# Kernel tuning notes

Measured on AMD Instinct MI355X. Metric: run time of the kernel, lower is better.

The kernel has to match this reference:

```python
import jax, jax.numpy as jnp
import numpy as np

MARKER = 50251
BETA_FLOOR = 0.1
LOCAL_SCALE = 0.3
EPS = 1e-6
WINDOW = 256

B, T, D, H, K, V = 4, 1024, 1024, 16, 64, 64
HD = D // H  # SWA head dim


def setup_inputs() -> dict:
    key = jax.random.key(0)
    ks = jax.random.split(key, 16)
    p = lambda i, shape: jax.random.normal(ks[i], shape, jnp.float32) * 0.02
    return dict(
        x=jax.random.normal(ks[0], (B, T, D), jnp.float32),
        initial_state=jnp.zeros((B, H, K, V), jnp.float32),
        W_k=p(1, (D, H * K)),
        W_v=p(2, (D, H * V)),
        W_gdn_o=p(3, (H * V, D)),
        W_beta=p(4, (D, H)), b_beta=jnp.full((H,), -2.0, jnp.float32),
        W_g=p(5, (D, H)), b_g=jnp.full((H,), 2.0, jnp.float32),
        W_lq=p(6, (D, D)), W_lk=p(7, (D, D)), W_lv=p(8, (D, D)),
        W_swa_o=p(9, (D, D)),
        W_ret_o=p(10, (H * V, D)),
        W_gate=p(11, (D, H)), b_gate=jnp.ones((H,), jnp.float32),
        norm_w=jnp.ones((D,), jnp.float32),
        input_ids=jax.random.randint(ks[12], (B, T), 0, 50257, jnp.int32),
    )


def _delta_scan(k, v, beta, g, S0):
    # gated delta rule:  Sd = g_t * S_{t-1};  S_t = Sd + beta_t * k_t (v_t - k_t Sd);  o_t = k_t S_t
    # k:[B,Tm,H,K]  v:[B,Tm,H,V]  beta,g:[B,Tm,H]  S0:[B,H,K,V]
    def step(S, inp):
        kt, vt, bt, gt = inp  # [B,H,K],[B,H,V],[B,H],[B,H]
        Sd = gt[..., None, None] * S
        err = vt - jnp.einsum('bhk,bhkv->bhv', kt, Sd)
        Sn = Sd + bt[..., None, None] * (kt[..., None] * err[:, :, None, :])
        ot = jnp.einsum('bhk,bhkv->bhv', kt, Sn)
        return Sn, ot
    Sf, o = jax.lax.scan(step, S0, (k.transpose(1, 0, 2, 3), v.transpose(1, 0, 2, 3),
                                    beta.transpose(1, 0, 2), g.transpose(1, 0, 2)))
    return o.transpose(1, 0, 2, 3), Sf  # [B,Tm,H,V], [B,H,K,V]


def _forward(x, initial_state, W_k, W_v, W_gdn_o, W_beta, b_beta, W_g, b_g,
             W_lq, W_lk, W_lv, W_swa_o, W_ret_o, W_gate, b_gate, norm_w, input_ids):
    # RMSNorm
    rms = jnp.sqrt(jnp.mean(x * x, axis=-1, keepdims=True) + EPS)
    xn = x / rms * norm_w

    # shared L2-normalized keys and values
    k_shared = (xn @ W_k).reshape(B, T, H, K)
    k_shared = k_shared / jnp.maximum(jnp.linalg.norm(k_shared, axis=-1, keepdims=True), 1e-12)
    v_full = (xn @ W_v).reshape(B, T, H, V)

    # shifted-value GDN inputs (predict next token's value)
    k = k_shared[:, :-1]
    v = v_full[:, 1:]
    beta = jax.nn.sigmoid(xn[:, :-1] @ W_beta + b_beta)  # [B,T-1,H]
    g = jax.nn.sigmoid(xn[:, :-1] @ W_g + b_g)
    marker = (input_ids[:, :-1] == MARKER)[..., None]
    beta = beta * (BETA_FLOOR + (1.0 - BETA_FLOOR) * marker.astype(beta.dtype))

    o, Sf = _delta_scan(k, v, beta, g, initial_state)
    gdn_out = jnp.concatenate([jnp.zeros((B, 1, H, V), o.dtype), o], axis=1)
    gdn_out = gdn_out.reshape(B, T, H * V) @ W_gdn_o  # [B,T,D]

    # sliding-window attention (fallback masked-softmax path)
    q = (xn @ W_lq).reshape(B, T, H, HD).transpose(0, 2, 1, 3)
    kl = (xn @ W_lk).reshape(B, T, H, HD).transpose(0, 2, 1, 3)
    vl = (xn @ W_lv).reshape(B, T, H, HD).transpose(0, 2, 1, 3)
    scale = K ** (-0.5)
    i = jnp.arange(T)[:, None]
    j = jnp.arange(T)[None, :]
    allowed = (j <= i) & (j >= i - WINDOW)  # causal within window
    attn = jnp.einsum('bhqd,bhkd->bhqk', q, kl) * scale
    attn = jnp.where(allowed, attn, -jnp.inf)
    probs = jax.nn.softmax(attn, axis=-1)
    local = jnp.einsum('bhqk,bhkd->bhqd', probs, vl).transpose(0, 2, 1, 3).reshape(B, T, D)
    local_out = LOCAL_SCALE * (local @ W_swa_o)  # eval mode

    # retrieval from final state with shared keys as queries
    retrieved = jnp.einsum('bhkv,bthk->bthv', Sf, k_shared).reshape(B, T, H * V)
    retrieval_out = retrieved @ W_ret_o
    gate = jax.nn.sigmoid(xn @ W_gate + b_gate)  # [B,T,H]
    retrieval_out = jnp.mean(gate, axis=-1, keepdims=True) * retrieval_out

    return x + gdn_out + local_out + retrieval_out


def reference(x, initial_state, W_k, W_v, W_gdn_o, W_beta, b_beta, W_g, b_g,
              W_lq, W_lk, W_lv, W_swa_o, W_ret_o, W_gate, b_gate, norm_w, input_ids):
    return _forward(x, initial_state, W_k, W_v, W_gdn_o, W_beta, b_beta, W_g, b_g,
                    W_lq, W_lk, W_lv, W_swa_o, W_ret_o, W_gate, b_gate, norm_w, input_ids)
```

## Files before the change

### kernel.cpp

```cpp
#include <hip/hip_runtime.h>
#include <hip/hip_bf16.h>

#define BB 4
#define TT 1024
#define DD 1024
#define HH 16
#define KK 64
#define VV 64
#define WIN 256
#define MARKER_ID 50251
#define PSA 5120
#define PSB 3072
#define NPROJ 5248

typedef short bfrag8 __attribute__((ext_vector_type(8)));
typedef float f32x4 __attribute__((ext_vector_type(4)));

static __device__ __forceinline__ unsigned short f2bf(float f) {
  __hip_bfloat16 h = __float2bfloat16(f);
  union { __hip_bfloat16 h; unsigned short u; } cv;
  cv.h = h;
  return cv.u;
}
static __device__ __forceinline__ float bf2f(unsigned short u) {
  union { unsigned int i; float f; } c;
  c.i = ((unsigned int)u) << 16;
  return c.f;
}
static __device__ __forceinline__ void gld_lds16(const unsigned short* g,
                                                 unsigned short* l) {
  __builtin_amdgcn_global_load_lds(
      (const __attribute__((address_space(1))) void*)g,
      (__attribute__((address_space(3))) void*)l, 16, 0, 0);
}

static __device__ __forceinline__ void rmsnorm_body(
    int row, const float* __restrict__ x, const float* __restrict__ nw,
    unsigned short* __restrict__ xnb, float* red) {
  int tid = threadIdx.x;
  const float4* xr = (const float4*)(x + (size_t)row * DD);
  float4 v = xr[tid];
  float ss = v.x * v.x + v.y * v.y + v.z * v.z + v.w * v.w;
#pragma unroll
  for (int off = 32; off; off >>= 1) ss += __shfl_xor(ss, off);
  int wid = tid >> 6;
  if ((tid & 63) == 0) red[wid] = ss;
  __syncthreads();
  float tot = red[0] + red[1] + red[2] + red[3];
  float inv = 1.0f / sqrtf(tot * (1.0f / DD) + 1e-6f);
  const float4* wr = (const float4*)nw;
  float4 wv = wr[tid];
  ushort4 o;
  o.x = f2bf(v.x * inv * wv.x);
  o.y = f2bf(v.y * inv * wv.y);
  o.z = f2bf(v.z * inv * wv.z);
  o.w = f2bf(v.w * inv * wv.w);
  *(ushort4*)&xnb[(size_t)row * DD + tid * 4] = o;
}

static __device__ __forceinline__ void convert_body(
    int xb, int yb, int zb, const float* W0, const float* W1, const float* W2,
    const float* W3, const float* W4, const float* W5, const float* W6,
    const float* W7, const float* Wb, const float* Wg, const float* Wgt,
    unsigned short* C5, unsigned short* C3, float (*Ts)[68]) {
  int tid = threadIdx.x;
  if (zb == 8) {
    if (xb != 0) return;
    int k0 = yb * 64;
    for (int e = tid; e < 3 * 16 * 64; e += 256) {
      int w = e >> 10;
      int h = (e >> 6) & 15;
      int kk = e & 63;
      const float* Ws = (w == 0) ? Wb : (w == 1) ? Wg : Wgt;
      C5[(size_t)(5120 + w * 16 + h) * 1024 + k0 + kk] =
          f2bf(Ws[(size_t)(k0 + kk) * 16 + h]);
    }
    for (int e = tid; e < 80 * 64; e += 256) {
      int r = e >> 6, kk = e & 63;
      C5[(size_t)(5168 + r) * 1024 + k0 + kk] = 0;
    }
    return;
  }
  const float* W;
  unsigned short* T;
  int stride;
  float scale = 1.f;
  switch (zb) {
    case 0: W = W0; T = C5 + 0 * 1024 * 1024; stride = 1024; break;
    case 1: W = W1; T = C5 + 1 * 1024 * 1024; stride = 1024; break;
    case 2: W = W2; T = C5 + 2 * 1024 * 1024; stride = 1024; break;
    case 3: W = W3; T = C5 + 3 * 1024 * 1024; stride = 1024; break;
    case 4: W = W4; T = C5 + 4 * 1024 * 1024; stride = 1024; break;
    case 5: W = W5; T = C3 + 0; stride = PSB; break;
    case 6: W = W6; T = C3 + 1024; stride = PSB; scale = 0.3f; break;
    default: W = W7; T = C3 + 2048; stride = PSB; break;
  }
  int n0 = xb * 64, k0 = yb * 64;
#pragma unroll
  for (int p = 0; p < 4; ++p) {
    int e = p * 256 + tid;
    int k = e >> 4, nq = e & 15;
    float4 w = *(const float4*)&W[(size_t)(k0 + k) * 1024 + n0 + nq * 4];
    Ts[nq * 4 + 0][k] = w.x;
    Ts[nq * 4 + 1][k] = w.y;
    Ts[nq * 4 + 2][k] = w.z;
    Ts[nq * 4 + 3][k] = w.w;
  }
  __syncthreads();
#pragma unroll
  for (int p = 0; p < 4; ++p) {
    int e = p * 256 + tid;
    int n = e >> 4, kq = e & 15;
    float4 v = *(const float4*)&Ts[n][kq * 4];
    ushort4 u;
    u.x = f2bf(v.x * scale);
    u.y = f2bf(v.y * scale);
    u.z = f2bf(v.z * scale);
    u.w = f2bf(v.w * scale);
    *(ushort4*)&T[(size_t)(n0 + n) * stride + k0 + kq * 4] = u;
  }
}

__global__ __launch_bounds__(256) void prep_kernel(
    const float* __restrict__ x, const float* __restrict__ nw,
    unsigned short* __restrict__ xnb, const float* W0, const float* W1,
    const float* W2, const float* W3, const float* W4, const float* W5,
    const float* W6, const float* W7, const float* Wb, const float* Wg,
    const float* Wgt, unsigned short* C5, unsigned short* C3) {
  __shared__ __align__(16) float Ts[64][68];
  int f = blockIdx.x;
  if (f < 4096) {
    rmsnorm_body(f, x, nw, xnb, &Ts[0][0]);
  } else {
    int c = f - 4096;
    convert_body(c & 15, (c >> 4) & 15, c >> 8, W0, W1, W2, W3, W4, W5, W6, W7,
                 Wb, Wg, Wgt, C5, C3, Ts);
  }
}

__global__ __launch_bounds__(256) void gemm_out_kernel(
    const unsigned short* __restrict__ A, const unsigned short* __restrict__ BT,
    float* __restrict__ C, const float* __restrict__ addp, int M, int N,
    int K) {
  __shared__ unsigned short As[2][128][32];
  __shared__ unsigned short Bs[2][64][32];
  int flat = blockIdx.y * gridDim.x + blockIdx.x;
  int xcd = flat & 7, local = flat >> 3;
  int m0 = (xcd * 4 + (local & 3)) * 128;
  int n0 = (local >> 2) * 64;
  int tid = threadIdx.x;
  int wave = tid >> 6, lane = tid & 63;
  int wm = wave * 32;
  int r16 = lane & 15, quad = lane >> 4;
  int lrow = lane >> 2, lcol = (lane & 3) * 8;

  f32x4 acc[2][4];
#pragma unroll
  for (int i = 0; i < 2; ++i)
#pragma unroll
    for (int j = 0; j < 4; ++j) acc[i][j] = {0.f, 0.f, 0.f, 0.f};

  auto STAGE = [&](int buf, int kt) {
#pragma unroll
    for (int q = 0; q < 2; ++q) {
      int rb = (wave * 2 + q) * 16;
      gld_lds16(&A[(size_t)(m0 + rb + lrow) * K + kt + lcol], &As[buf][rb][0]);
    }
    {
      int rb = wave * 16;
      gld_lds16(&BT[(size_t)(n0 + rb + lrow) * K + kt + lcol], &Bs[buf][rb][0]);
    }
  };
  auto COMPUTE = [&](int buf) {
    bfrag8 af[2], bq[4];
#pragma unroll
    for (int i = 0; i < 2; ++i)
      af[i] = *(const bfrag8*)&As[buf][wm + i * 16 + r16][quad * 8];
#pragma unroll
    for (int j = 0; j < 4; ++j)
      bq[j] = *(const bfrag8*)&Bs[buf][j * 16 + r16][quad * 8];
#pragma unroll
    for (int i = 0; i < 2; ++i)
#pragma unroll
      for (int j = 0; j < 4; ++j)
        acc[i][j] = __builtin_amdgcn_mfma_f32_16x16x32_bf16(af[i], bq[j],
                                                            acc[i][j], 0, 0, 0);
  };

  STAGE(0, 0);
  STAGE(1, 32);
  asm volatile("s_waitcnt vmcnt(3)" ::: "memory");
  __builtin_amdgcn_s_barrier();
  __builtin_amdgcn_sched_barrier(0);

  int cur = 0;
  for (int kt = 64; kt < K; kt += 32) {
    COMPUTE(cur);
    __builtin_amdgcn_s_barrier();
    STAGE(cur, kt);
    asm volatile("s_waitcnt vmcnt(3)" ::: "memory");
    __builtin_amdgcn_s_barrier();
    __builtin_amdgcn_sched_barrier(0);
    cur ^= 1;
  }
  COMPUTE(cur);
  asm volatile("s_waitcnt vmcnt(0)" ::: "memory");
  __builtin_amdgcn_s_barrier();
  __builtin_amdgcn_sched_barrier(0);
  COMPUTE(cur ^ 1);

#pragma unroll
  for (int i = 0; i < 2; ++i) {
#pragma unroll
    for (int r = 0; r < 4; ++r) {
      int row = m0 + wm + i * 16 + quad * 4 + r;
#pragma unroll
      for (int j = 0; j < 4; ++j) {
        int col = n0 + j * 16 + r16;
        size_t idx = (size_t)row * N + col;
        C[idx] = addp[idx] + acc[i][j][r];
      }
    }
  }
}

__global__ __launch_bounds__(256, 4) void gemm_proj_kernel(
    const unsigned short* __restrict__ A, const unsigned short* __restrict__ BT,
    unsigned short* __restrict__ PALL, float* __restrict__ SPRJ) {
  const int K = 1024;
  __shared__ unsigned short As[2][128][32];
  __shared__ unsigned short Bs[2][128][32];
  int flat = blockIdx.y * gridDim.x + blockIdx.x;
  int xcd = flat & 7, local = flat >> 3;
  int mi = local & 3, ni = local >> 2;
  int m0 = (xcd * 4 + mi) * 128;
  int n0 = ni * 128;
  int tid = threadIdx.x;
  int wave = tid >> 6, lane = tid & 63;
  int wm = (wave & 1) * 64, wn = (wave >> 1) * 64;
  int r16 = lane & 15, quad = lane >> 4;
  int lrow = lane >> 2, lcol = (lane & 3) * 8;

  f32x4 acc[4][4];
#pragma unroll
  for (int i = 0; i < 4; ++i)
#pragma unroll
    for (int j = 0; j < 4; ++j) acc[i][j] = {0.f, 0.f, 0.f, 0.f};

#pragma unroll
  for (int q = 0; q < 2; ++q) {
    int rb = (wave * 2 + q) * 16;
    gld_lds16(&A[(size_t)(m0 + rb + lrow) * K + lcol], &As[0][rb][0]);
    gld_lds16(&BT[(size_t)(n0 + rb + lrow) * K + lcol], &Bs[0][rb][0]);
  }
  __syncthreads();

  int cur = 0;
  for (int kt = 32; kt < K; kt += 32) {
#pragma unroll
    for (int q = 0; q < 2; ++q) {
      int rb = (wave * 2 + q) * 16;
      gld_lds16(&A[(size_t)(m0 + rb + lrow) * K + kt + lcol],
                &As[cur ^ 1][rb][0]);
      gld_lds16(&BT[(size_t)(n0 + rb + lrow) * K + kt + lcol],
                &Bs[cur ^ 1][rb][0]);
    }
    bfrag8 af[4], bq[4];
#pragma unroll
    for (int i = 0; i < 4; ++i) {
      af[i] = *(const bfrag8*)&As[cur][wm + i * 16 + r16][quad * 8];
      bq[i] = *(const bfrag8*)&Bs[cur][wn + i * 16 + r16][quad * 8];
    }
#pragma unroll
    for (int i = 0; i < 4; ++i)
#pragma unroll
      for (int j = 0; j < 4; ++j)
        acc[i][j] = __builtin_amdgcn_mfma_f32_16x16x32_bf16(af[i], bq[j],
                                                            acc[i][j], 0, 0, 0);
    __syncthreads();
    cur ^= 1;
  }
  {
    bfrag8 af[4], bq[4];
#pragma unroll
    for (int i = 0; i < 4; ++i) {
      af[i] = *(const bfrag8*)&As[cur][wm + i * 16 + r16][quad * 8];
      bq[i] = *(const bfrag8*)&Bs[cur][wn + i * 16 + r16][quad * 8];
    }
#pragma unroll
    for (int i = 0; i < 4; ++i)
#pragma unroll
      for (int j = 0; j < 4; ++j)
        acc[i][j] = __builtin_amdgcn_mfma_f32_16x16x32_bf16(af[i], bq[j],
                                                            acc[i][j], 0, 0, 0);
  }
  bool gates = (n0 >= 5120);
#pragma unroll
  for (int i = 0; i < 4; ++i) {
#pragma unroll
    for (int r = 0; r < 4; ++r) {
      int row = m0 + wm + i * 16 + quad * 4 + r;
#pragma unroll
      for (int j = 0; j < 4; ++j) {
        int col = n0 + wn + j * 16 + r16;
        if (!gates)
          PALL[(size_t)row * PSA + col] = f2bf(acc[i][j][r]);
        else
          SPRJ[(size_t)row * 128 + col - 5120] = acc[i][j][r];
      }
    }
  }
}

__global__ __launch_bounds__(256) void ng_kernel(
    unsigned short* __restrict__ pall, const float* __restrict__ SPRJ,
    const float* __restrict__ bb, const float* __restrict__ bg,
    const float* __restrict__ bgt, const int* __restrict__ ids,
    float* __restrict__ beta, float* __restrict__ g, float* __restrict__ mg) {
  int f = blockIdx.x;
  if (f < 16384) {
    int w = f * 4 + (threadIdx.x >> 6);
    int lane = threadIdx.x & 63;
    size_t addr = (size_t)(w >> 4) * PSA + (w & 15) * 64 + lane;
    float v = bf2f(pall[addr]);
    float ss = v * v;
#pragma unroll
    for (int off = 32; off; off >>= 1) ss += __shfl_xor(ss, off);
    float n = sqrtf(ss);
    n = fmaxf(n, 1e-12f);
    pall[addr] = f2bf(v / n);
  } else {
    int row = (f - 16384) * 4 + (threadIdx.x >> 6);
    int lane = threadIdx.x & 63;
    if (lane < 48) {
      int h = lane & 15;
      float v = SPRJ[(size_t)row * 128 + lane];
      float bias = (lane < 16) ? bb[h] : (lane < 32) ? bg[h] : bgt[h];
      float s = 1.f / (1.f + __expf(-(v + bias)));
      if (lane < 16) {
        float mk = (ids[row] == MARKER_ID) ? 1.f : 0.1f;
        beta[(size_t)row * 16 + h] = s * mk;
      } else if (lane < 32) {
        g[(size_t)row * 16 + h] = s;
      } else {
        float sum = s;
#pragma unroll
        for (int off = 1; off < 16; off <<= 1) sum += __shfl_xor(sum, off);
        if (lane == 32) mg[row] = sum * (1.f / 16.f);
      }
    }
  }
}

__global__ __launch_bounds__(256) void attn_mfma_kernel(
    const unsigned short* __restrict__ PALL, unsigned short* __restrict__ ACAT) {
  __shared__ unsigned short Qs[64][72];
  __shared__ unsigned short Ks[64][72];
  __shared__ unsigned short Vt[64][72];
  __shared__ unsigned short Ps[64][72];
  int qb = blockIdx.x * 64;
  int bh = blockIdx.y;
  int h = bh & 15, b = bh >> 4;
  int tid = threadIdx.x, lane = tid & 63, wave = tid >> 6;
  int r16 = lane & 15, quad = lane >> 4;
  int m0w = wave * 16;
  const unsigned short* Qg = PALL + (size_t)b * TT * PSA + 2048 + h * 64;
  const unsigned short* Kg = Qg + 1024;
  const unsigned short* Vg = Qg + 2048;
  int sr = tid >> 2, sq = tid & 3;
  int kt0 = qb - (int)WIN;
  if (kt0 < 0) kt0 = 0;

  uint4 kr0, kr1;
  union { uint4 u4[2]; unsigned short s[16]; } vr;
  {
    *(uint4*)&Qs[sr][sq * 16] =
        *(const uint4*)&Qg[(size_t)(qb + sr) * PSA + sq * 16];
    *(uint4*)&Qs[sr][sq * 16 + 8] =
        *(const uint4*)&Qg[(size_t)(qb + sr) * PSA + sq * 16 + 8];
    kr0 = *(const uint4*)&Kg[(size_t)(kt0 + sr) * PSA + sq * 16];
    kr1 = *(const uint4*)&Kg[(size_t)(kt0 + sr) * PSA + sq * 16 + 8];
    vr.u4[0] = *(const uint4*)&Vg[(size_t)(kt0 + sr) * PSA + sq * 16];
    vr.u4[1] = *(const uint4*)&Vg[(size_t)(kt0 + sr) * PSA + sq * 16 + 8];
  }
  __syncthreads();
  bfrag8 af0 = *(const bfrag8*)&Qs[m0w + r16][quad * 8];
  bfrag8 af1 = *(const bfrag8*)&Qs[m0w + r16][quad * 8 + 32];
  {
    *(uint4*)&Ks[sr][sq * 16] = kr0;
    *(uint4*)&Ks[sr][sq * 16 + 8] = kr1;
#pragma unroll
    for (int i = 0; i < 16; ++i) Vt[sq * 16 + i][sr] = vr.s[i];
  }
  __syncthreads();

  float m[4], l[4];
  f32x4 o[4];
#pragma unroll
  for (int r = 0; r < 4; ++r) {
    m[r] = -1e30f;
    l[r] = 0.f;
    o[r] = {0.f, 0.f, 0.f, 0.f};
  }

  for (int kt = kt0; kt <= qb; kt += 64) {
    bool more = (kt + 64 <= qb);
    if (more) {
      kr0 = *(const uint4*)&Kg[(size_t)(kt + 64 + sr) * PSA + sq * 16];
      kr1 = *(const uint4*)&Kg[(size_t)(kt + 64 + sr) * PSA + sq * 16 + 8];
      vr.u4[0] = *(const uint4*)&Vg[(size_t)(kt + 64 + sr) * PSA + sq * 16];
      vr.u4[1] = *(const uint4*)&Vg[(size_t)(kt + 64 + sr) * PSA + sq * 16 + 8];
    }
    f32x4 s[4];
#pragma unroll
    for (int j = 0; j < 4; ++j) s[j] = {0.f, 0.f, 0.f, 0.f};
#pragma unroll
    for (int j = 0; j < 4; ++j) {
      bfrag8 b0 = *(const bfrag8*)&Ks[j * 16 + r16][quad * 8];
      bfrag8 b1 = *(const bfrag8*)&Ks[j * 16 + r16][quad * 8 + 32];
      s[j] = __builtin_amdgcn_mfma_f32_16x16x32_bf16(af0, b0, s[j], 0, 0, 0);
      s[j] = __builtin_amdgcn_mfma_f32_16x16x32_bf16(af1, b1, s[j], 0, 0, 0);
    }
    bool oldest = (kt == qb - (int)WIN);
    bool newest = (kt == qb);
#pragma unroll
    for (int r = 0; r < 4; ++r) {
      int il = m0w + quad * 4 + r;
      float sv[4];
#pragma unroll
      for (int j = 0; j < 4; ++j) {
        int jl = j * 16 + r16;
        float v = s[j][r] * 0.125f;
        if (oldest && jl < il) v = -1e30f;
        if (newest && jl > il) v = -1e30f;
        sv[j] = v;
      }
      float mx = fmaxf(fmaxf(sv[0], sv[1]), fmaxf(sv[2], sv[3]));
#pragma unroll
      for (int off = 1; off < 16; off <<= 1) mx = fmaxf(mx, __shfl_xor(mx, off));
      float mn = fmaxf(m[r], mx);
      float al = __expf(m[r] - mn);
      m[r] = mn;
      float rs = 0.f;
#pragma unroll
      for (int j = 0; j < 4; ++j) {
        float p = __expf(sv[j] - mn);
        rs += p;
        Ps[il][j * 16 + r16] = f2bf(p);
      }
#pragma unroll
      for (int off = 1; off < 16; off <<= 1) rs += __shfl_xor(rs, off);
      l[r] = l[r] * al + rs;
#pragma unroll
      for (int j = 0; j < 4; ++j) o[j][r] *= al;
    }
    bfrag8 pa0 = *(const bfrag8*)&Ps[m0w + r16][quad * 8];
    bfrag8 pa1 = *(const bfrag8*)&Ps[m0w + r16][quad * 8 + 32];
#pragma unroll
    for (int j = 0; j < 4; ++j) {
      bfrag8 v0 = *(const bfrag8*)&Vt[j * 16 + r16][quad * 8];
      bfrag8 v1 = *(const bfrag8*)&Vt[j * 16 + r16][quad * 8 + 32];
      o[j] = __builtin_amdgcn_mfma_f32_16x16x32_bf16(pa0, v0, o[j], 0, 0, 0);
      o[j] = __builtin_amdgcn_mfma_f32_16x16x32_bf16(pa1, v1, o[j], 0, 0, 0);
    }
    if (more) {
      __syncthreads();
      *(uint4*)&Ks[sr][sq * 16] = kr0;
      *(uint4*)&Ks[sr][sq * 16 + 8] = kr1;
#pragma unroll
      for (int i = 0; i < 16; ++i) Vt[sq * 16 + i][sr] = vr.s[i];
      __syncthreads();
    }
  }
#pragma unroll
  for (int r = 0; r < 4; ++r) {
    int row = m0w + quad * 4 + r;
    float inv = 1.f / l[r];
#pragma unroll
    for (int j = 0; j < 4; ++j) {
      ACAT[((size_t)(b * TT + qb + row)) * PSB + 1024 + h * 64 + j * 16 + r16] =
          f2bf(o[j][r] * inv);
    }
  }
}

__global__ __launch_bounds__(256) void scan_phaseA(
    const unsigned short* __restrict__ PALL, const float* __restrict__ beta,
    const float* __restrict__ g, unsigned short* __restrict__ UFg,
    unsigned short* __restrict__ Zg, unsigned short* __restrict__ Pg,
    unsigned short* __restrict__ Qg, float* __restrict__ Ag) {
  __shared__ unsigned short Kc[64][72];
  __shared__ unsigned short KTb[64][72];
  __shared__ float Vc[64][68];
  __shared__ float Msv[64][68];
  __shared__ unsigned short UFT[64][72];
  __shared__ unsigned short ZTl[64][72];
  __shared__ float aArr[64], iaArr[64], bArr[64], baArr[64], sKT[64];
  __shared__ float aCs;

  int c = blockIdx.x, bh = blockIdx.y;
  int b = bh >> 4, h = bh & 15;
  int tc = c * 64;
  int tid = threadIdx.x, lane = tid & 63, wave = tid >> 6;
  int r16 = lane & 15, quad = lane >> 4;
  int m0w = wave * 16;
  size_t bhc = (size_t)bh * 16 + c;

  const unsigned short* kbase = PALL + ((size_t)b * TT) * PSA + h * 64;
  const unsigned short* vbase = kbase + 1024;
  const float* bbase = beta + ((size_t)b * TT) * HH + h;
  const float* gbase = g + ((size_t)b * TT) * HH + h;

  if (tid < 64) {
    int ts = tc + tid;
    bool pad = (ts > 1022);
    float gv = pad ? 1.f : gbase[(size_t)ts * HH];
    float bv = pad ? 0.f : bbase[(size_t)ts * HH];
    float p = gv;
#pragma unroll
    for (int o = 1; o < 64; o <<= 1) {
      float t = __shfl_up(p, o);
      if (lane >= o) p *= t;
    }
    aArr[tid] = p;
    iaArr[tid] = 1.f / p;
    bArr[tid] = bv;
    baArr[tid] = bv * p;
    float aC = __shfl(p, 63);
    sKT[tid] = aC / p;
    if (tid == 0) aCs = aC;
    Ag[bhc * 64 + tid] = p;
  }
  __syncthreads();
  {
    int r = tid >> 2, q = tid & 3;
    int ts = tc + r;
    float skt = sKT[r];
    union { uint4 u4[2]; unsigned short s[16]; } kv;
    kv.u4[0] = *(const uint4*)&kbase[(size_t)ts * PSA + q * 16];
    kv.u4[1] = *(const uint4*)&kbase[(size_t)ts * PSA + q * 16 + 8];
    *(uint4*)&Kc[r][q * 16] = kv.u4[0];
    *(uint4*)&Kc[r][q * 16 + 8] = kv.u4[1];
#pragma unroll
    for (int i = 0; i < 16; ++i)
      KTb[q * 16 + i][r] = f2bf(bf2f(kv.s[i]) * skt);
    if (ts <= 1022) {
      union { uint4 u4[2]; unsigned short s[16]; } vv;
      vv.u4[0] = *(const uint4*)&vbase[(size_t)(ts + 1) * PSA + q * 16];
      vv.u4[1] = *(const uint4*)&vbase[(size_t)(ts + 1) * PSA + q * 16 + 8];
#pragma unroll
      for (int i = 0; i < 16; ++i) Vc[r][q * 16 + i] = bf2f(vv.s[i]);
    } else {
#pragma unroll
      for (int i = 0; i < 16; ++i) Vc[r][q * 16 + i] = 0.f;
    }
  }
  __syncthreads();
  {
    bfrag8 af0 = *(const bfrag8*)&Kc[m0w + r16][quad * 8];
    bfrag8 af1 = *(const bfrag8*)&Kc[m0w + r16][quad * 8 + 32];
    f32x4 acc1[4];
#pragma unroll
    for (int j = 0; j < 4; ++j) acc1[j] = {0.f, 0.f, 0.f, 0.f};
#pragma unroll
    for (int j = 0; j < 4; ++j) {
      bfrag8 k0 = *(const bfrag8*)&Kc[j * 16 + r16][quad * 8];
      bfrag8 k1 = *(const bfrag8*)&Kc[j * 16 + r16][quad * 8 + 32];
      acc1[j] = __builtin_amdgcn_mfma_f32_16x16x32_bf16(af0, k0, acc1[j], 0, 0, 0);
      acc1[j] = __builtin_amdgcn_mfma_f32_16x16x32_bf16(af1, k1, acc1[j], 0, 0, 0);
    }
#pragma unroll
    for (int j = 0; j < 4; ++j) {
#pragma unroll
      for (int r = 0; r < 4; ++r) {
        int row = m0w + quad * 4 + r;
        int col = j * 16 + r16;
        Msv[row][col] =
            (col < row) ? bArr[row] * aArr[row] * iaArr[col] * acc1[j][r] : 0.f;
      }
    }
  }
  __syncthreads();
  if (wave < 2) {
    float u[64];
    if (wave == 0) {
#pragma unroll
      for (int t = 0; t < 64; ++t) u[t] = bArr[t] * Vc[t][lane];
    } else {
#pragma unroll
      for (int t = 0; t < 64; ++t) u[t] = baArr[t] * bf2f(Kc[t][lane]);
    }
#pragma unroll
    for (int t = 1; t < 64; ++t) {
      float a0 = 0.f, a1 = 0.f, a2 = 0.f, a3 = 0.f;
#pragma unroll
      for (int s4 = 0; s4 * 4 < t; ++s4) {
        float4 mr = *(const float4*)&Msv[t][s4 * 4];
        a0 = fmaf(mr.x, u[s4 * 4 + 0], a0);
        a1 = fmaf(mr.y, u[s4 * 4 + 1], a1);
        a2 = fmaf(mr.z, u[s4 * 4 + 2], a2);
        a3 = fmaf(mr.w, u[s4 * 4 + 3], a3);
      }
      u[t] -= (a0 + a1) + (a2 + a3);
    }
    unsigned short* Tls = (wave == 0) ? &UFT[lane][0] : &ZTl[lane][0];
#pragma unroll
    for (int t2 = 0; t2 < 32; ++t2) {
      unsigned int pk = (unsigned int)f2bf(u[2 * t2]) |
                        ((unsigned int)f2bf(u[2 * t2 + 1]) << 16);
      *(unsigned int*)&Tls[2 * t2] = pk;
    }
    unsigned short* Gn = (wave == 0) ? UFg : Zg;
#pragma unroll
    for (int t = 0; t < 64; ++t) {
      Gn[(bhc * 64 + t) * 64 + lane] = f2bf(u[t]);
    }
  }
  __syncthreads();
  {
    bfrag8 af0 = *(const bfrag8*)&KTb[m0w + r16][quad * 8];
    bfrag8 af1 = *(const bfrag8*)&KTb[m0w + r16][quad * 8 + 32];
    f32x4 accp[4], accq[4];
#pragma unroll
    for (int j = 0; j < 4; ++j) {
      accp[j] = {0.f, 0.f, 0.f, 0.f};
      accq[j] = {0.f, 0.f, 0.f, 0.f};
    }
#pragma unroll
    for (int j = 0; j < 4; ++j) {
      bfrag8 z0 = *(const bfrag8*)&ZTl[j * 16 + r16][quad * 8];
      bfrag8 z1 = *(const bfrag8*)&ZTl[j * 16 + r16][quad * 8 + 32];
      accp[j] = __builtin_amdgcn_mfma_f32_16x16x32_bf16(af0, z0, accp[j], 0, 0, 0);
      accp[j] = __builtin_amdgcn_mfma_f32_16x16x32_bf16(af1, z1, accp[j], 0, 0, 0);
      bfrag8 u0 = *(const bfrag8*)&UFT[j * 16 + r16][quad * 8];
      bfrag8 u1 = *(const bfrag8*)&UFT[j * 16 + r16][quad * 8 + 32];
      accq[j] = __builtin_amdgcn_mfma_f32_16x16x32_bf16(af0, u0, accq[j], 0, 0, 0);
      accq[j] = __builtin_amdgcn_mfma_f32_16x16x32_bf16(af1, u1, accq[j], 0, 0, 0);
    }
    float aC = aCs;
#pragma unroll
    for (int j = 0; j < 4; ++j) {
#pragma unroll
      for (int r = 0; r < 4; ++r) {
        int row = m0w + quad * 4 + r;
        int col = j * 16 + r16;
        float pv = ((row == col) ? aC : 0.f) - accp[j][r];
        Pg[bhc * 4096 + (size_t)row * 64 + col] = f2bf(pv);
        Qg[bhc * 4096 + (size_t)row * 64 + col] = f2bf(accq[j][r]);
      }
    }
  }
}

__global__ __launch_bounds__(256) void scan_phaseB(
    const float* __restrict__ S0, const unsigned short* __restrict__ Pg,
    const unsigned short* __restrict__ Qg, unsigned short* __restrict__ SinTg,
    float* __restrict__ Sf, unsigned short* __restrict__ ACAT) {
  __shared__ unsigned short STb[64][72];
  __shared__ unsigned short Pl[64][72];
  int bh = blockIdx.x;
  int b = bh >> 4, h = bh & 15;
  int tid = threadIdx.x, lane = tid & 63, wave = tid >> 6;
  int r16 = lane & 15, quad = lane >> 4;
  int m0w = wave * 16;
  int rr = tid >> 2, qq = tid & 3;
  {
    const float* s0p = S0 + (size_t)bh * 4096;
#pragma unroll
    for (int i = 0; i < 4; ++i) {
      float4 sv = *(const float4*)&s0p[rr * 64 + qq * 16 + i * 4];
      STb[qq * 16 + i * 4 + 0][rr] = f2bf(sv.x);
      STb[qq * 16 + i * 4 + 1][rr] = f2bf(sv.y);
      STb[qq * 16 + i * 4 + 2][rr] = f2bf(sv.z);
      STb[qq * 16 + i * 4 + 3][rr] = f2bf(sv.w);
    }
    if (tid < 64) ACAT[((size_t)b * TT) * PSB + h * 64 + tid] = 0;
  }
  for (int c = 0; c < 16; ++c) {
    size_t bhc = (size_t)bh * 16 + c;
    __syncthreads();
    {
      uint4 s0v = *(const uint4*)&STb[rr][qq * 16];
      uint4 s1v = *(const uint4*)&STb[rr][qq * 16 + 8];
      *(uint4*)&SinTg[bhc * 4096 + (size_t)rr * 64 + qq * 16] = s0v;
      *(uint4*)&SinTg[bhc * 4096 + (size_t)rr * 64 + qq * 16 + 8] = s1v;
      uint4 p0 = *(const uint4*)&Pg[bhc * 4096 + (size_t)rr * 64 + qq * 16];
      uint4 p1 = *(const uint4*)&Pg[bhc * 4096 + (size_t)rr * 64 + qq * 16 + 8];
      *(uint4*)&Pl[rr][qq * 16] = p0;
      *(uint4*)&Pl[rr][qq * 16 + 8] = p1;
    }
    __syncthreads();
    f32x4 acc[4];
#pragma unroll
    for (int j = 0; j < 4; ++j) acc[j] = {0.f, 0.f, 0.f, 0.f};
    {
      bfrag8 af0 = *(const bfrag8*)&Pl[m0w + r16][quad * 8];
      bfrag8 af1 = *(const bfrag8*)&Pl[m0w + r16][quad * 8 + 32];
#pragma unroll
      for (int j = 0; j < 4; ++j) {
        bfrag8 s0v = *(const bfrag8*)&STb[j * 16 + r16][quad * 8];
        bfrag8 s1v = *(const bfrag8*)&STb[j * 16 + r16][quad * 8 + 32];
        acc[j] = __builtin_amdgcn_mfma_f32_16x16x32_bf16(af0, s0v, acc[j], 0, 0, 0);
        acc[j] = __builtin_amdgcn_mfma_f32_16x16x32_bf16(af1, s1v, acc[j], 0, 0, 0);
      }
    }
    float snew[4][4];
#pragma unroll
    for (int j = 0; j < 4; ++j) {
#pragma unroll
      for (int r = 0; r < 4; ++r) {
        int row = m0w + quad * 4 + r;
        int col = j * 16 + r16;
        snew[j][r] = acc[j][r] + bf2f(Qg[bhc * 4096 + (size_t)row * 64 + col]);
      }
    }
    __syncthreads();
#pragma unroll
    for (int j = 0; j < 4; ++j) {
#pragma unroll
      for (int r = 0; r < 4; ++r) {
        int row = m0w + quad * 4 + r;
        int col = j * 16 + r16;
        STb[col][row] = f2bf(snew[j][r]);
        if (c == 15) Sf[(size_t)bh * 4096 + (size_t)row * 64 + col] = snew[j][r];
      }
    }
  }
}

union Sm3 {
  struct {
    unsigned short Kc[64][72], SvT[64][72], Zl[64][72], Ufl[64][72],
        Wl[64][72], UTl[64][72];
    float aA[64], iaA[64];
  } sc;
  struct { float Sfs[64][64]; } rt;
};

static __device__ void scanC_body(
    int c, int bh, const unsigned short* __restrict__ PALL,
    const unsigned short* __restrict__ UFg,
    const unsigned short* __restrict__ Zg,
    const unsigned short* __restrict__ SinTg, const float* __restrict__ Ag,
    unsigned short* __restrict__ ACAT, Sm3& sm) {
  auto& Kc = sm.sc.Kc;
  auto& SvT = sm.sc.SvT;
  auto& Zl = sm.sc.Zl;
  auto& Ufl = sm.sc.Ufl;
  auto& Wl = sm.sc.Wl;
  auto& UTl = sm.sc.UTl;
  auto& aA = sm.sc.aA;
  auto& iaA = sm.sc.iaA;

  int b = bh >> 4, h = bh & 15;
  int tc = c * 64;
  int tid = threadIdx.x, lane = tid & 63, wave = tid >> 6;
  int r16 = lane & 15, quad = lane >> 4;
  int m0w = wave * 16;
  size_t bhc = (size_t)bh * 16 + c;
  const unsigned short* kbase = PALL + ((size_t)b * TT) * PSA + h * 64;

  if (tid < 64) {
    float av = Ag[bhc * 64 + tid];
    aA[tid] = av;
    iaA[tid] = 1.f / av;
  }
  {
    int r = tid >> 2, q = tid & 3;
    int ts = tc + r;
    *(uint4*)&Kc[r][q * 16] = *(const uint4*)&kbase[(size_t)ts * PSA + q * 16];
    *(uint4*)&Kc[r][q * 16 + 8] =
        *(const uint4*)&kbase[(size_t)ts * PSA + q * 16 + 8];
    uint4 sv0 = *(const uint4*)&SinTg[bhc * 4096 + (size_t)r * 64 + q * 16];
    uint4 sv1 = *(const uint4*)&SinTg[bhc * 4096 + (size_t)r * 64 + q * 16 + 8];
    *(uint4*)&SvT[r][q * 16] = sv0;
    *(uint4*)&SvT[r][q * 16 + 8] = sv1;
    uint4 zv0 = *(const uint4*)&Zg[(bhc * 64 + r) * 64 + q * 16];
    uint4 zv1 = *(const uint4*)&Zg[(bhc * 64 + r) * 64 + q * 16 + 8];
    *(uint4*)&Zl[r][q * 16] = zv0;
    *(uint4*)&Zl[r][q * 16 + 8] = zv1;
    uint4 uv0 = *(const uint4*)&UFg[(bhc * 64 + r) * 64 + q * 16];
    uint4 uv1 = *(const uint4*)&UFg[(bhc * 64 + r) * 64 + q * 16 + 8];
    *(uint4*)&Ufl[r][q * 16] = uv0;
    *(uint4*)&Ufl[r][q * 16 + 8] = uv1;
  }
  __syncthreads();
  float op[4][4];
  {
    bfrag8 af0 = *(const bfrag8*)&Kc[m0w + r16][quad * 8];
    bfrag8 af1 = *(const bfrag8*)&Kc[m0w + r16][quad * 8 + 32];
    bfrag8 zf0 = *(const bfrag8*)&Zl[m0w + r16][quad * 8];
    bfrag8 zf1 = *(const bfrag8*)&Zl[m0w + r16][quad * 8 + 32];
    f32x4 acc1[4], acc2[4], acc3[4];
#pragma unroll
    for (int j = 0; j < 4; ++j) {
      acc1[j] = {0.f, 0.f, 0.f, 0.f};
      acc2[j] = {0.f, 0.f, 0.f, 0.f};
      acc3[j] = {0.f, 0.f, 0.f, 0.f};
    }
#pragma unroll
    for (int j = 0; j < 4; ++j) {
      bfrag8 k0 = *(const bfrag8*)&Kc[j * 16 + r16][quad * 8];
      bfrag8 k1 = *(const bfrag8*)&Kc[j * 16 + r16][quad * 8 + 32];
      acc1[j] = __builtin_amdgcn_mfma_f32_16x16x32_bf16(af0, k0, acc1[j], 0, 0, 0);
      acc1[j] = __builtin_amdgcn_mfma_f32_16x16x32_bf16(af1, k1, acc1[j], 0, 0, 0);
      bfrag8 s0 = *(const bfrag8*)&SvT[j * 16 + r16][quad * 8];
      bfrag8 s1 = *(const bfrag8*)&SvT[j * 16 + r16][quad * 8 + 32];
      acc3[j] = __builtin_amdgcn_mfma_f32_16x16x32_bf16(af0, s0, acc3[j], 0, 0, 0);
      acc3[j] = __builtin_amdgcn_mfma_f32_16x16x32_bf16(af1, s1, acc3[j], 0, 0, 0);
      acc2[j] = __builtin_amdgcn_mfma_f32_16x16x32_bf16(zf0, s0, acc2[j], 0, 0, 0);
      acc2[j] = __builtin_amdgcn_mfma_f32_16x16x32_bf16(zf1, s1, acc2[j], 0, 0, 0);
    }
#pragma unroll
    for (int j = 0; j < 4; ++j) {
#pragma unroll
      for (int r = 0; r < 4; ++r) {
        int row = m0w + quad * 4 + r;
        int col = j * 16 + r16;
        Wl[row][col] = (col <= row) ? f2bf(aA[row] * iaA[col] * acc1[j][r])
                                    : (unsigned short)0;
        float uval = bf2f(Ufl[row][col]) - acc2[j][r];
        UTl[col][row] = f2bf(uval);
        op[j][r] = aA[row] * acc3[j][r];
      }
    }
  }
  __syncthreads();
  {
    bfrag8 wf0 = *(const bfrag8*)&Wl[m0w + r16][quad * 8];
    bfrag8 wf1 = *(const bfrag8*)&Wl[m0w + r16][quad * 8 + 32];
    f32x4 acc4[4];
#pragma unroll
    for (int j = 0; j < 4; ++j) acc4[j] = {0.f, 0.f, 0.f, 0.f};
#pragma unroll
    for (int j = 0; j < 4; ++j) {
      bfrag8 u0 = *(const bfrag8*)&UTl[j * 16 + r16][quad * 8];
      bfrag8 u1 = *(const bfrag8*)&UTl[j * 16 + r16][quad * 8 + 32];
      acc4[j] = __builtin_amdgcn_mfma_f32_16x16x32_bf16(wf0, u0, acc4[j], 0, 0, 0);
      acc4[j] = __builtin_amdgcn_mfma_f32_16x16x32_bf16(wf1, u1, acc4[j], 0, 0, 0);
    }
#pragma unroll
    for (int j = 0; j < 4; ++j) {
#pragma unroll
      for (int r = 0; r < 4; ++r) {
        int row = m0w + quad * 4 + r;
        int col = j * 16 + r16;
        int ts = tc + row;
        if (ts < 1023) {
          ACAT[((size_t)b * TT + ts + 1) * PSB + h * 64 + col] =
              f2bf(op[j][r] + acc4[j][r]);
        }
      }
    }
  }
}

static __device__ void retrieve_body(
    int cx, int bh, const unsigned short* __restrict__ PALL,
    const float* __restrict__ Sf, const float* __restrict__ mg,
    unsigned short* __restrict__ ACAT, Sm3& sm) {
  auto& Sfs = sm.rt.Sfs;
  int tc = cx * 64;
  int b = bh >> 4, h = bh & 15;
  int tid = threadIdx.x, lane = tid & 63, wave = tid >> 6;
  const float* sfp = Sf + (size_t)bh * 4096;
#pragma unroll
  for (int i = 0; i < 4; ++i) {
    int e = tid + i * 256;
    ((float4*)&Sfs[0][0])[e] = ((const float4*)sfp)[e];
  }
  __syncthreads();
  const unsigned short* kb = PALL + ((size_t)b * TT) * PSA + h * 64;
#pragma unroll 2
  for (int ti = 0; ti < 16; ++ti) {
    int t = tc + wave * 16 + ti;
    size_t bt = (size_t)b * TT + t;
    float kl = bf2f(kb[(size_t)t * PSA + lane]);
    float a0 = 0.f, a1 = 0.f, a2 = 0.f, a3 = 0.f;
#pragma unroll
    for (int k = 0; k < 64; k += 4) {
      a0 = fmaf(__shfl(kl, k + 0), Sfs[k + 0][lane], a0);
      a1 = fmaf(__shfl(kl, k + 1), Sfs[k + 1][lane], a1);
      a2 = fmaf(__shfl(kl, k + 2), Sfs[k + 2][lane], a2);
      a3 = fmaf(__shfl(kl, k + 3), Sfs[k + 3][lane], a3);
    }
    float acc = (a0 + a1) + (a2 + a3);
    ACAT[bt * PSB + 2048 + h * 64 + lane] = f2bf(acc * mg[bt]);
  }
}

__global__ __launch_bounds__(256) void scanC_retr_kernel(
    const unsigned short* __restrict__ PALL,
    const unsigned short* __restrict__ UFg,
    const unsigned short* __restrict__ Zg,
    const unsigned short* __restrict__ SinTg, const float* __restrict__ Ag,
    const float* __restrict__ Sf, const float* __restrict__ mg,
    unsigned short* __restrict__ ACAT) {
  __shared__ Sm3 sm;
  int bx = blockIdx.x;
  int sel = bx & 1, idx = bx >> 1;
  int cx = idx & 15, bh = idx >> 4;
  if (sel == 0)
    scanC_body(cx, bh, PALL, UFg, Zg, SinTg, Ag, ACAT, sm);
  else
    retrieve_body(cx, bh, PALL, Sf, mg, ACAT, sm);
}

extern "C" void kernel_launch(void* const* d_in, const int* in_sizes, int n_in,
                              void* d_out, int out_size, void* d_ws,
                              size_t ws_size, hipStream_t stream) {
  (void)in_sizes; (void)n_in; (void)out_size; (void)ws_size;
  const float* x       = (const float*)d_in[0];
  const float* S0      = (const float*)d_in[1];
  const float* W_k     = (const float*)d_in[2];
  const float* W_v     = (const float*)d_in[3];
  const float* W_gdn_o = (const float*)d_in[4];
  const float* b_beta  = (const float*)d_in[6];
  const float* W_beta  = (const float*)d_in[5];
  const float* W_g     = (const float*)d_in[7];
  const float* b_g     = (const float*)d_in[8];
  const float* W_lq    = (const float*)d_in[9];
  const float* W_lk    = (const float*)d_in[10];
  const float* W_lv    = (const float*)d_in[11];
  const float* W_swa_o = (const float*)d_in[12];
  const float* W_ret_o = (const float*)d_in[13];
  const float* W_gate  = (const float*)d_in[14];
  const float* b_gate  = (const float*)d_in[15];
  const float* norm_w  = (const float*)d_in[16];
  const int*   ids     = (const int*)d_in[17];
  float* out = (float*)d_out;

  char* ws = (char*)d_ws;
  size_t off = 0;
  auto allocf = [&](size_t n) {
    float* p = (float*)(ws + off);
    off += n * sizeof(float);
    return p;
  };
  auto allocu = [&](size_t n) {
    unsigned short* p = (unsigned short*)(ws + off);
    off += n * sizeof(unsigned short);
    return p;
  };
  const int M = BB * TT;
  unsigned short* XNb    = allocu((size_t)M * DD);
  unsigned short* PALL   = allocu((size_t)M * PSA);
  unsigned short* ACAT   = allocu((size_t)M * PSB);
  float*          SPRJ   = allocf((size_t)M * 128);
  unsigned short* WTcat5 = allocu((size_t)NPROJ * 1024);
  unsigned short* WTcat3 = allocu((size_t)1024 * PSB);
  float* BETA = allocf((size_t)M * HH);
  float* Gg   = allocf((size_t)M * HH);
  float* MG   = allocf((size_t)M);
  float* SF   = allocf((size_t)BB * HH * KK * VV);
  const size_t CH = (size_t)BB * HH * 16 * 64 * 64;
  unsigned short* UFg   = allocu(CH);
  unsigned short* Zg    = allocu(CH);
  unsigned short* Pg    = allocu(CH);
  unsigned short* Qg    = allocu(CH);
  unsigned short* SinTg = allocu(CH);
  float* Ag = allocf((size_t)BB * HH * 16 * 64);

  prep_kernel<<<6400, 256, 0, stream>>>(x, norm_w, XNb, W_k, W_v, W_lq, W_lk,
                                        W_lv, W_gdn_o, W_swa_o, W_ret_o,
                                        W_beta, W_g, W_gate, WTcat5, WTcat3);

  gemm_proj_kernel<<<dim3(41, 32), 256, 0, stream>>>(XNb, WTcat5, PALL, SPRJ);

  ng_kernel<<<17408, 256, 0, stream>>>(PALL, SPRJ, b_beta, b_g, b_gate, ids,
                                       BETA, Gg, MG);

  scan_phaseA<<<dim3(16, BB * HH), 256, 0, stream>>>(PALL, BETA, Gg, UFg, Zg,
                                                     Pg, Qg, Ag);
  scan_phaseB<<<BB * HH, 256, 0, stream>>>(S0, Pg, Qg, SinTg, SF, ACAT);

  attn_mfma_kernel<<<dim3(TT / 64, BB * HH), 256, 0, stream>>>(PALL, ACAT);

  scanC_retr_kernel<<<2048, 256, 0, stream>>>(PALL, UFg, Zg, SinTg, Ag, SF, MG,
                                              ACAT);

  gemm_out_kernel<<<dim3(16, 32), 256, 0, stream>>>(ACAT, WTcat3, out, x, M, DD,
                                                    3072);
}
```

Measured before the change: 423.7 us.

## Fuse sliding-window attention into combined scanC/retrieval tail kernel

Merges the separate attention kernel into the existing scanC/retrieval kernel, giving a single 3072-block launch that interleaves attention, scan-C and retrieval blocks by blockIdx mod 3. This removes one kernel launch and its tail gap, and lets independent work overlap on the GPU. To keep the shared union small enough for 4 blocks per CU (launch_bounds 256,4), scanC now reads Z fragments and UF values straight from global memory instead of staging them in LDS. The risks are uncoalesced or redundant global reads in scanC and heterogeneous block types causing register pressure or imbalance.

```diff
diff --git a/kernel.cpp b/kernel.cpp
--- a/kernel.cpp
+++ b/kernel.cpp
@@ -352,138 +352,6 @@
   }
 }
 
-__global__ __launch_bounds__(256) void attn_mfma_kernel(
-    const unsigned short* __restrict__ PALL, unsigned short* __restrict__ ACAT) {
-  __shared__ unsigned short Qs[64][72];
-  __shared__ unsigned short Ks[64][72];
-  __shared__ unsigned short Vt[64][72];
-  __shared__ unsigned short Ps[64][72];
-  int qb = blockIdx.x * 64;
-  int bh = blockIdx.y;
-  int h = bh & 15, b = bh >> 4;
-  int tid = threadIdx.x, lane = tid & 63, wave = tid >> 6;
-  int r16 = lane & 15, quad = lane >> 4;
-  int m0w = wave * 16;
-  const unsigned short* Qg = PALL + (size_t)b * TT * PSA + 2048 + h * 64;
-  const unsigned short* Kg = Qg + 1024;
-  const unsigned short* Vg = Qg + 2048;
-  int sr = tid >> 2, sq = tid & 3;
-  int kt0 = qb - (int)WIN;
-  if (kt0 < 0) kt0 = 0;
-
-  uint4 kr0, kr1;
-  union { uint4 u4[2]; unsigned short s[16]; } vr;
-  {
-    *(uint4*)&Qs[sr][sq * 16] =
-        *(const uint4*)&Qg[(size_t)(qb + sr) * PSA + sq * 16];
-    *(uint4*)&Qs[sr][sq * 16 + 8] =
-        *(const uint4*)&Qg[(size_t)(qb + sr) * PSA + sq * 16 + 8];
-    kr0 = *(const uint4*)&Kg[(size_t)(kt0 + sr) * PSA + sq * 16];
-    kr1 = *(const uint4*)&Kg[(size_t)(kt0 + sr) * PSA + sq * 16 + 8];
-    vr.u4[0] = *(const uint4*)&Vg[(size_t)(kt0 + sr) * PSA + sq * 16];
-    vr.u4[1] = *(const uint4*)&Vg[(size_t)(kt0 + sr) * PSA + sq * 16 + 8];
-  }
-  __syncthreads();
-  bfrag8 af0 = *(const bfrag8*)&Qs[m0w + r16][quad * 8];
-  bfrag8 af1 = *(const bfrag8*)&Qs[m0w + r16][quad * 8 + 32];
-  {
-    *(uint4*)&Ks[sr][sq * 16] = kr0;
-    *(uint4*)&Ks[sr][sq * 16 + 8] = kr1;
-#pragma unroll
-    for (int i = 0; i < 16; ++i) Vt[sq * 16 + i][sr] = vr.s[i];
-  }
-  __syncthreads();
-
-  float m[4], l[4];
-  f32x4 o[4];
-#pragma unroll
-  for (int r = 0; r < 4; ++r) {
-    m[r] = -1e30f;
-    l[r] = 0.f;
-    o[r] = {0.f, 0.f, 0.f, 0.f};
-  }
-
-  for (int kt = kt0; kt <= qb; kt += 64) {
-    bool more = (kt + 64 <= qb);
-    if (more) {
-      kr0 = *(const uint4*)&Kg[(size_t)(kt + 64 + sr) * PSA + sq * 16];
-      kr1 = *(const uint4*)&Kg[(size_t)(kt + 64 + sr) * PSA + sq * 16 + 8];
-      vr.u4[0] = *(const uint4*)&Vg[(size_t)(kt + 64 + sr) * PSA + sq * 16];
-      vr.u4[1] = *(const uint4*)&Vg[(size_t)(kt + 64 + sr) * PSA + sq * 16 + 8];
-    }
-    f32x4 s[4];
-#pragma unroll
-    for (int j = 0; j < 4; ++j) s[j] = {0.f, 0.f, 0.f, 0.f};
-#pragma unroll
-    for (int j = 0; j < 4; ++j) {
-      bfrag8 b0 = *(const bfrag8*)&Ks[j * 16 + r16][quad * 8];
-      bfrag8 b1 = *(const bfrag8*)&Ks[j * 16 + r16][quad * 8 + 32];
-      s[j] = __builtin_amdgcn_mfma_f32_16x16x32_bf16(af0, b0, s[j], 0, 0, 0);
-      s[j] = __builtin_amdgcn_mfma_f32_16x16x32_bf16(af1, b1, s[j], 0, 0, 0);
-    }
-    bool oldest = (kt == qb - (int)WIN);
-    bool newest = (kt == qb);
-#pragma unroll
-    for (int r = 0; r < 4; ++r) {
-      int il = m0w + quad * 4 + r;
-      float sv[4];
-#pragma unroll
-      for (int j = 0; j < 4; ++j) {
-        int jl = j * 16 + r16;
-        float v = s[j][r] * 0.125f;
-        if (oldest && jl < il) v = -1e30f;
-        if (newest && jl > il) v = -1e30f;
-        sv[j] = v;
-      }
-      float mx = fmaxf(fmaxf(sv[0], sv[1]), fmaxf(sv[2], sv[3]));
-#pragma unroll
-      for (int off = 1; off < 16; off <<= 1) mx = fmaxf(mx, __shfl_xor(mx, off));
-      float mn = fmaxf(m[r], mx);
-      float al = __expf(m[r] - mn);
-      m[r] = mn;
-      float rs = 0.f;
-#pragma unroll
-      for (int j = 0; j < 4; ++j) {
-        float p = __expf(sv[j] - mn);
-        rs += p;
-        Ps[il][j * 16 + r16] = f2bf(p);
-      }
-#pragma unroll
-      for (int off = 1; off < 16; off <<= 1) rs += __shfl_xor(rs, off);
-      l[r] = l[r] * al + rs;
-#pragma unroll
-      for (int j = 0; j < 4; ++j) o[j][r] *= al;
-    }
-    bfrag8 pa0 = *(const bfrag8*)&Ps[m0w + r16][quad * 8];
-    bfrag8 pa1 = *(const bfrag8*)&Ps[m0w + r16][quad * 8 + 32];
-#pragma unroll
-    for (int j = 0; j < 4; ++j) {
-      bfrag8 v0 = *(const bfrag8*)&Vt[j * 16 + r16][quad * 8];
-      bfrag8 v1 = *(const bfrag8*)&Vt[j * 16 + r16][quad * 8 + 32];
-      o[j] = __builtin_amdgcn_mfma_f32_16x16x32_bf16(pa0, v0, o[j], 0, 0, 0);
-      o[j] = __builtin_amdgcn_mfma_f32_16x16x32_bf16(pa1, v1, o[j], 0, 0, 0);
-    }
-    if (more) {
-      __syncthreads();
-      *(uint4*)&Ks[sr][sq * 16] = kr0;
-      *(uint4*)&Ks[sr][sq * 16 + 8] = kr1;
-#pragma unroll
-      for (int i = 0; i < 16; ++i) Vt[sq * 16 + i][sr] = vr.s[i];
-      __syncthreads();
-    }
-  }
-#pragma unroll
-  for (int r = 0; r < 4; ++r) {
-    int row = m0w + quad * 4 + r;
-    float inv = 1.f / l[r];
-#pragma unroll
-    for (int j = 0; j < 4; ++j) {
-      ACAT[((size_t)(b * TT + qb + row)) * PSB + 1024 + h * 64 + j * 16 + r16] =
-          f2bf(o[j][r] * inv);
-    }
-  }
-}
-
 __global__ __launch_bounds__(256) void scan_phaseA(
     const unsigned short* __restrict__ PALL, const float* __restrict__ beta,
     const float* __restrict__ g, unsigned short* __restrict__ UFg,
@@ -728,25 +596,155 @@
   }
 }
 
-union Sm3 {
+union SmF {
+  struct { unsigned short Qs[64][72], Ks[64][72], Vt[64][72], Ps[64][72]; } at;
   struct {
-    unsigned short Kc[64][72], SvT[64][72], Zl[64][72], Ufl[64][72],
-        Wl[64][72], UTl[64][72];
+    unsigned short Kc[64][72], SvT[64][72], Wl[64][72], UTl[64][72];
     float aA[64], iaA[64];
   } sc;
   struct { float Sfs[64][64]; } rt;
 };
+
+static __device__ void attn_body(int qi, const unsigned short* __restrict__ PALL,
+                                 unsigned short* __restrict__ ACAT, SmF& sm) {
+  auto& Qs = sm.at.Qs;
+  auto& Ks = sm.at.Ks;
+  auto& Vt = sm.at.Vt;
+  auto& Ps = sm.at.Ps;
+  int qb = (qi & 15) * 64;
+  int bh = qi >> 4;
+  int h = bh & 15, b = bh >> 4;
+  int tid = threadIdx.x, lane = tid & 63, wave = tid >> 6;
+  int r16 = lane & 15, quad = lane >> 4;
+  int m0w = wave * 16;
+  const unsigned short* Qg = PALL + (size_t)b * TT * PSA + 2048 + h * 64;
+  const unsigned short* Kg = Qg + 1024;
+  const unsigned short* Vg = Qg + 2048;
+  int sr = tid >> 2, sq = tid & 3;
+  int kt0 = qb - (int)WIN;
+  if (kt0 < 0) kt0 = 0;
+
+  uint4 kr0, kr1;
+  union { uint4 u4[2]; unsigned short s[16]; } vr;
+  {
+    *(uint4*)&Qs[sr][sq * 16] =
+        *(const uint4*)&Qg[(size_t)(qb + sr) * PSA + sq * 16];
+    *(uint4*)&Qs[sr][sq * 16 + 8] =
+        *(const uint4*)&Qg[(size_t)(qb + sr) * PSA + sq * 16 + 8];
+    kr0 = *(const uint4*)&Kg[(size_t)(kt0 + sr) * PSA + sq * 16];
+    kr1 = *(const uint4*)&Kg[(size_t)(kt0 + sr) * PSA + sq * 16 + 8];
+    vr.u4[0] = *(const uint4*)&Vg[(size_t)(kt0 + sr) * PSA + sq * 16];
+    vr.u4[1] = *(const uint4*)&Vg[(size_t)(kt0 + sr) * PSA + sq * 16 + 8];
+  }
+  __syncthreads();
+  bfrag8 af0 = *(const bfrag8*)&Qs[m0w + r16][quad * 8];
+  bfrag8 af1 = *(const bfrag8*)&Qs[m0w + r16][quad * 8 + 32];
+  {
+    *(uint4*)&Ks[sr][sq * 16] = kr0;
+    *(uint4*)&Ks[sr][sq * 16 + 8] = kr1;
+#pragma unroll
+    for (int i = 0; i < 16; ++i) Vt[sq * 16 + i][sr] = vr.s[i];
+  }
+  __syncthreads();
+
+  float m[4], l[4];
+  f32x4 o[4];
+#pragma unroll
+  for (int r = 0; r < 4; ++r) {
+    m[r] = -1e30f;
+    l[r] = 0.f;
+    o[r] = {0.f, 0.f, 0.f, 0.f};
+  }
+
+  for (int kt = kt0; kt <= qb; kt += 64) {
+    bool more = (kt + 64 <= qb);
+    if (more) {
+      kr0 = *(const uint4*)&Kg[(size_t)(kt + 64 + sr) * PSA + sq * 16];
+      kr1 = *(const uint4*)&Kg[(size_t)(kt + 64 + sr) * PSA + sq * 16 + 8];
+      vr.u4[0] = *(const uint4*)&Vg[(size_t)(kt + 64 + sr) * PSA + sq * 16];
+      vr.u4[1] = *(const uint4*)&Vg[(size_t)(kt + 64 + sr) * PSA + sq * 16 + 8];
+    }
+    f32x4 s[4];
+#pragma unroll
+    for (int j = 0; j < 4; ++j) s[j] = {0.f, 0.f, 0.f, 0.f};
+#pragma unroll
+    for (int j = 0; j < 4; ++j) {
+      bfrag8 b0 = *(const bfrag8*)&Ks[j * 16 + r16][quad * 8];
+      bfrag8 b1 = *(const bfrag8*)&Ks[j * 16 + r16][quad * 8 + 32];
+      s[j] = __builtin_amdgcn_mfma_f32_16x16x32_bf16(af0, b0, s[j], 0, 0, 0);
+      s[j] = __builtin_amdgcn_mfma_f32_16x16x32_bf16(af1, b1, s[j], 0, 0, 0);
+    }
+    bool oldest = (kt == qb - (int)WIN);
+    bool newest = (kt == qb);
+#pragma unroll
+    for (int r = 0; r < 4; ++r) {
+      int il = m0w + quad * 4 + r;
+      float sv[4];
+#pragma unroll
+      for (int j = 0; j < 4; ++j) {
+        int jl = j * 16 + r16;
+        float v = s[j][r] * 0.125f;
+        if (oldest && jl < il) v = -1e30f;
+        if (newest && jl > il) v = -1e30f;
+        sv[j] = v;
+      }
+      float mx = fmaxf(fmaxf(sv[0], sv[1]), fmaxf(sv[2], sv[3]));
+#pragma unroll
+      for (int off = 1; off < 16; off <<= 1) mx = fmaxf(mx, __shfl_xor(mx, off));
+      float mn = fmaxf(m[r], mx);
+      float al = __expf(m[r] - mn);
+      m[r] = mn;
+      float rs = 0.f;
+#pragma unroll
+      for (int j = 0; j < 4; ++j) {
+        float p = __expf(sv[j] - mn);
+        rs += p;
+        Ps[il][j * 16 + r16] = f2bf(p);
+      }
+#pragma unroll
+      for (int off = 1; off < 16; off <<= 1) rs += __shfl_xor(rs, off);
+      l[r] = l[r] * al + rs;
+#pragma unroll
+      for (int j = 0; j < 4; ++j) o[j][r] *= al;
+    }
+    bfrag8 pa0 = *(const bfrag8*)&Ps[m0w + r16][quad * 8];
+    bfrag8 pa1 = *(const bfrag8*)&Ps[m0w + r16][quad * 8 + 32];
+#pragma unroll
+    for (int j = 0; j < 4; ++j) {
+      bfrag8 v0 = *(const bfrag8*)&Vt[j * 16 + r16][quad * 8];
+      bfrag8 v1 = *(const bfrag8*)&Vt[j * 16 + r16][quad * 8 + 32];
+      o[j] = __builtin_amdgcn_mfma_f32_16x16x32_bf16(pa0, v0, o[j], 0, 0, 0);
+      o[j] = __builtin_amdgcn_mfma_f32_16x16x32_bf16(pa1, v1, o[j], 0, 0, 0);
+    }
+    if (more) {
+      __syncthreads();
+      *(uint4*)&Ks[sr][sq * 16] = kr0;
+      *(uint4*)&Ks[sr][sq * 16 + 8] = kr1;
+#pragma unroll
+      for (int i = 0; i < 16; ++i) Vt[sq * 16 + i][sr] = vr.s[i];
+      __syncthreads();
+    }
+  }
+#pragma unroll
+  for (int r = 0; r < 4; ++r) {
+    int row = m0w + quad * 4 + r;
+    float inv = 1.f / l[r];
+#pragma unroll
+    for (int j = 0; j < 4; ++j) {
+      ACAT[((size_t)(b * TT + qb + row)) * PSB + 1024 + h * 64 + j * 16 + r16] =
+          f2bf(o[j][r] * inv);
+    }
+  }
+}
 
 static __device__ void scanC_body(
     int c, int bh, const unsigned short* __restrict__ PALL,
     const unsigned short* __restrict__ UFg,
     const unsigned short* __restrict__ Zg,
     const unsigned short* __restrict__ SinTg, const float* __restrict__ Ag,
-    unsigned short* __restrict__ ACAT, Sm3& sm) {
+    unsigned short* __restrict__ ACAT, SmF& sm) {
   auto& Kc = sm.sc.Kc;
   auto& SvT = sm.sc.SvT;
-  auto& Zl = sm.sc.Zl;
-  auto& Ufl = sm.sc.Ufl;
   auto& Wl = sm.sc.Wl;
   auto& UTl = sm.sc.UTl;
   auto& aA = sm.sc.aA;
@@ -775,22 +773,15 @@
     uint4 sv1 = *(const uint4*)&SinTg[bhc * 4096 + (size_t)r * 64 + q * 16 + 8];
     *(uint4*)&SvT[r][q * 16] = sv0;
     *(uint4*)&SvT[r][q * 16 + 8] = sv1;
-    uint4 zv0 = *(const uint4*)&Zg[(bhc * 64 + r) * 64 + q * 16];
-    uint4 zv1 = *(const uint4*)&Zg[(bhc * 64 + r) * 64 + q * 16 + 8];
-    *(uint4*)&Zl[r][q * 16] = zv0;
-    *(uint4*)&Zl[r][q * 16 + 8] = zv1;
-    uint4 uv0 = *(const uint4*)&UFg[(bhc * 64 + r) * 64 + q * 16];
-    uint4 uv1 = *(const uint4*)&UFg[(bhc * 64 + r) * 64 + q * 16 + 8];
-    *(uint4*)&Ufl[r][q * 16] = uv0;
-    *(uint4*)&Ufl[r][q * 16 + 8] = uv1;
-  }
+  }
+  bfrag8 zf0 = *(const bfrag8*)&Zg[(bhc * 64 + m0w + r16) * 64 + quad * 8];
+  bfrag8 zf1 =
+      *(const bfrag8*)&Zg[(bhc * 64 + m0w + r16) * 64 + quad * 8 + 32];
   __syncthreads();
   float op[4][4];
   {
     bfrag8 af0 = *(const bfrag8*)&Kc[m0w + r16][quad * 8];
     bfrag8 af1 = *(const bfrag8*)&Kc[m0w + r16][quad * 8 + 32];
-    bfrag8 zf0 = *(const bfrag8*)&Zl[m0w + r16][quad * 8];
-    bfrag8 zf1 = *(const bfrag8*)&Zl[m0w + r16][quad * 8 + 32];
     f32x4 acc1[4], acc2[4], acc3[4];
 #pragma unroll
     for (int j = 0; j < 4; ++j) {
@@ -819,7 +810,7 @@
         int col = j * 16 + r16;
         Wl[row][col] = (col <= row) ? f2bf(aA[row] * iaA[col] * acc1[j][r])
                                     : (unsigned short)0;
-        float uval = bf2f(Ufl[row][col]) - acc2[j][r];
+        float uval = bf2f(UFg[(bhc * 64 + row) * 64 + col]) - acc2[j][r];
         UTl[col][row] = f2bf(uval);
         op[j][r] = aA[row] * acc3[j][r];
       }
@@ -858,7 +849,7 @@
 static __device__ void retrieve_body(
     int cx, int bh, const unsigned short* __restrict__ PALL,
     const float* __restrict__ Sf, const float* __restrict__ mg,
-    unsigned short* __restrict__ ACAT, Sm3& sm) {
+    unsigned short* __restrict__ ACAT, SmF& sm) {
   auto& Sfs = sm.rt.Sfs;
   int tc = cx * 64;
   int b = bh >> 4, h = bh & 15;
@@ -889,21 +880,24 @@
   }
 }
 
-__global__ __launch_bounds__(256) void scanC_retr_kernel(
+__global__ __launch_bounds__(256, 4) void tail3_kernel(
     const unsigned short* __restrict__ PALL,
     const unsigned short* __restrict__ UFg,
     const unsigned short* __restrict__ Zg,
     const unsigned short* __restrict__ SinTg, const float* __restrict__ Ag,
     const float* __restrict__ Sf, const float* __restrict__ mg,
     unsigned short* __restrict__ ACAT) {
-  __shared__ Sm3 sm;
+  __shared__ SmF sm;
   int bx = blockIdx.x;
-  int sel = bx & 1, idx = bx >> 1;
-  int cx = idx & 15, bh = idx >> 4;
-  if (sel == 0)
-    scanC_body(cx, bh, PALL, UFg, Zg, SinTg, Ag, ACAT, sm);
-  else
-    retrieve_body(cx, bh, PALL, Sf, mg, ACAT, sm);
+  int type = bx % 3;
+  int idx = bx / 3;
+  if (type == 0) {
+    attn_body(idx, PALL, ACAT, sm);
+  } else if (type == 1) {
+    scanC_body(idx & 15, idx >> 4, PALL, UFg, Zg, SinTg, Ag, ACAT, sm);
+  } else {
+    retrieve_body(idx & 15, idx >> 4, PALL, Sf, mg, ACAT, sm);
+  }
 }
 
 extern "C" void kernel_launch(void* const* d_in, const int* in_sizes, int n_in,
@@ -915,8 +909,8 @@
   const float* W_k     = (const float*)d_in[2];
   const float* W_v     = (const float*)d_in[3];
   const float* W_gdn_o = (const float*)d_in[4];
+  const float* W_beta  = (const float*)d_in[5];
   const float* b_beta  = (const float*)d_in[6];
-  const float* W_beta  = (const float*)d_in[5];
   const float* W_g     = (const float*)d_in[7];
   const float* b_g     = (const float*)d_in[8];
   const float* W_lq    = (const float*)d_in[9];
@@ -974,10 +968,8 @@
                                                      Pg, Qg, Ag);
   scan_phaseB<<<BB * HH, 256, 0, stream>>>(S0, Pg, Qg, SinTg, SF, ACAT);
 
-  attn_mfma_kernel<<<dim3(TT / 64, BB * HH), 256, 0, stream>>>(PALL, ACAT);
-
-  scanC_retr_kernel<<<2048, 256, 0, stream>>>(PALL, UFg, Zg, SinTg, Ag, SF, MG,
-                                              ACAT);
+  tail3_kernel<<<3072, 256, 0, stream>>>(PALL, UFg, Zg, SinTg, Ag, SF, MG,
+                                         ACAT);
 
   gemm_out_kernel<<<dim3(16, 32), 256, 0, stream>>>(ACAT, WTcat3, out, x, M, DD,
                                                     3072);
```

Result: slower. 463.9 us (+9.5%).
